# Kernel tuning notes

Hardware: AMD Instinct MI355X
Metric: run time of the kernel (lower is better)

The kernel has to match this reference:

```python
import jax, jax.numpy as jnp
import numpy as np

N_NODES = 50000
N_EDGES = 800000
D = 256          # in_features == out_features == num_classes
T = 4            # number of replicas / linear heads
NS = 64          # num_edges (hyperedges)


def setup_inputs() -> dict:
    key = jax.random.key(0)
    ks = jax.random.split(key, 10)
    s = D ** -0.5
    return {
        "edge_index": jax.random.randint(ks[0], (2, N_EDGES), 0, N_NODES, dtype=jnp.int64)
        if jax.config.jax_enable_x64 else jax.random.randint(ks[0], (2, N_EDGES), 0, N_NODES, dtype=jnp.int32),
        "features": jax.random.normal(ks[1], (N_NODES, D), jnp.float32),
        "lin_w": jax.random.normal(ks[2], (T, D, D), jnp.float32) * s,
        "lin_b": jax.random.normal(ks[3], (T, D), jnp.float32) * 0.01,
        "gcn0_w": jax.random.normal(ks[4], (D, D), jnp.float32) * s,
        "gcn0_b": jax.random.normal(ks[5], (D,), jnp.float32) * 0.01,
        "gcn1_w": jax.random.normal(ks[6], (D, D), jnp.float32) * s,
        "gcn1_b": jax.random.normal(ks[7], (D,), jnp.float32) * 0.01,
        "lin1_w": jax.random.normal(ks[8], (D, NS), jnp.float32) * s,
        "lin1_b": jax.random.normal(ks[9], (NS,), jnp.float32) * 0.01,
    }


def _l2_normalize(x, eps=1e-8):
    n = jnp.sqrt(jnp.sum(x * x, axis=-1, keepdims=True))
    return x / jnp.maximum(n, eps)


def reference(edge_index, features, lin_w, lin_b, gcn0_w, gcn0_b, gcn1_w, gcn1_b, lin1_w, lin1_b):
    num_nodes, d = features.shape
    t = lin_w.shape[0]
    ns = lin1_w.shape[1]
    scale = d ** -0.5  # out_features ** -0.5

    # t linear projections: (t, N, D)
    transformed = jnp.einsum('nd,tdk->tnk', features, lin_w) + lin_b[:, None, :]

    src, dst = edge_index[0], edge_index[1]
    # cosine similarity of features[src] vs each replica's transformed[dst]
    fs = _l2_normalize(features)[src]              # (E, D)
    tf_n = _l2_normalize(transformed)              # (t, N, D)
    sim = jnp.stack([jnp.sum(fs * tf_n[i][dst], axis=-1) for i in range(t)], axis=1)  # (E, t)
    best_idx = jnp.argmax(sim, axis=1)
    best_dst = dst + best_idx.astype(dst.dtype) * num_nodes

    # extra per-replica identity edges: node n -> node n + i*N, i in [0, t)
    ar = jnp.arange(num_nodes, dtype=src.dtype)
    extra_src = jnp.tile(ar, t)
    extra_dst = (ar[None, :] + (jnp.arange(t, dtype=src.dtype) * num_nodes)[:, None]).reshape(-1)

    src_all = jnp.concatenate([src, src, extra_src])
    dst_all = jnp.concatenate([dst, best_dst, extra_dst])
    n_total = (t + 1) * num_nodes

    # PyG gcn_norm: drop pre-existing self loops (weight 0), add one self loop per node,
    # symmetric normalization with degree from destination index.
    loops = jnp.arange(n_total, dtype=src.dtype)
    src2 = jnp.concatenate([src_all, loops])
    dst2 = jnp.concatenate([dst_all, loops])
    w2 = jnp.concatenate([jnp.where(src_all == dst_all, 0.0, 1.0).astype(features.dtype),
                          jnp.ones(n_total, features.dtype)])
    deg = jax.ops.segment_sum(w2, dst2, num_segments=n_total)
    dinv = jnp.where(deg > 0, jax.lax.rsqrt(deg), 0.0)
    norm = w2 * dinv[src2] * dinv[dst2]

    def gcn(x, W, b):
        xw = x @ W
        return jax.ops.segment_sum(norm[:, None] * xw[src2], dst2, num_segments=n_total) + b

    all_features = jnp.concatenate([features, transformed.reshape(t * num_nodes, d)], axis=0)
    # dropout is identity in eval mode
    h = jax.nn.relu(all_features)
    h = gcn(h, gcn0_w, gcn0_b)
    h = jax.nn.relu(h)
    all_features2 = gcn(h, gcn1_w, gcn1_b)          # ((t+1)N, D)
    logits = jax.nn.relu(all_features2) @ lin1_w + lin1_b  # ((t+1)N, NS)

    # H[n, c] counts how many of the (t+1) replicas assign node n to cluster c
    classes = jnp.argmax(logits.reshape(t + 1, num_nodes, ns), axis=-1)  # (t+1, N)
    H = jax.nn.one_hot(classes, ns, dtype=features.dtype).sum(axis=0)     # (N, NS)

    # hyperedge features: sum of all_features2 over base-replica nodes in each hyperedge
    mask = (H > 0).astype(features.dtype)                                  # (N, NS)
    hyperedge_features = mask.T @ all_features2[:num_nodes]                # (NS, D)

    dots = (all_features @ hyperedge_features.T) * scale                   # ((t+1)N, NS)
    return H, hyperedge_features, dots
```

## Files before the change

### kernel.cpp

```cpp
#include <hip/hip_runtime.h>

#define D 256
#define T 4
#define NS 64

typedef unsigned int uint32;
typedef short s16x8 __attribute__((ext_vector_type(8)));
typedef float f32x4 __attribute__((ext_vector_type(4)));

__device__ __forceinline__ float bflo(uint32 u) { return __uint_as_float(u << 16); }
__device__ __forceinline__ float bfhi(uint32 u) { return __uint_as_float(u & 0xffff0000u); }
__device__ __forceinline__ unsigned short f2bf(float x) {
    uint32 u = __float_as_uint(x);
    u = u + 0x7FFFu + ((u >> 16) & 1u);
    return (unsigned short)(u >> 16);
}
__device__ __forceinline__ uint32 pack2(float a, float b) {
    return (uint32)f2bf(a) | ((uint32)f2bf(b) << 16);
}
__device__ __forceinline__ uint32 relu2(uint32 u) {
    uint32 s = u & 0x80008000u;
    uint32 m = ((s >> 15) ^ 0x00010001u) * 0xFFFFu;
    return u & m;
}

__global__ void zero_kernel(uint32* __restrict__ p, long long n)
{
    long long i = (long long)blockIdx.x * blockDim.x + threadIdx.x;
    long long st = (long long)gridDim.x * blockDim.x;
    for (; i < n; i += st) p[i] = 0u;
}

__global__ void f2bf_kernel(const float* __restrict__ in, unsigned short* __restrict__ out,
                            long long n8)
{
    long long i = (long long)blockIdx.x * blockDim.x + threadIdx.x;
    long long st = (long long)gridDim.x * blockDim.x;
    for (; i < n8; i += st) {
        float4 a = *(const float4*)(in + i * 8);
        float4 b = *(const float4*)(in + i * 8 + 4);
        uint4 o;
        o.x = pack2(a.x, a.y); o.y = pack2(a.z, a.w);
        o.z = pack2(b.x, b.y); o.w = pack2(b.z, b.w);
        *(uint4*)(out + i * 8) = o;
    }
}

__global__ void wfrag_kernel(const float* __restrict__ g0, const float* __restrict__ g1,
                             const float* __restrict__ lw, unsigned short* __restrict__ out)
{
    int o = blockIdx.x * 256 + threadIdx.x;
    int mat = blockIdx.y;
    const float* W = (mat == 0) ? g0 : (mat == 1) ? g1 : (lw + (size_t)(mat - 2) * 65536);
    int j = o & 7, lane = (o >> 3) & 63, ks = (o >> 9) & 7, nt = o >> 12;
    int n15 = lane & 15, quad = lane >> 4;
    int k = ks * 32 + quad * 8 + j;
    int n = nt * 16 + n15;
    out[(size_t)mat * 65536 + o] = f2bf(W[(size_t)k * 256 + n]);
}

__global__ __launch_bounds__(256, 2)
void gemm_mfma(const unsigned short* __restrict__ A,
               const unsigned short* __restrict__ Wfrag,
               const float* __restrict__ bias,
               unsigned short* __restrict__ Cout,
               int M, int nStripes, int rowMul, int zRowAdd)
{
    __shared__ unsigned short Asm[64 * 264];
    int t = threadIdx.x, w = t >> 6, lane = t & 63;
    int n15 = lane & 15, quad = lane >> 4;
    int z = blockIdx.y;
    Wfrag += (size_t)z * 65536;
    bias  += (size_t)z * 256;

    s16x8 bfr[4][8];
#pragma unroll
    for (int nt = 0; nt < 4; nt++)
#pragma unroll
        for (int ks = 0; ks < 8; ks++)
            bfr[nt][ks] = *(const s16x8*)(Wfrag +
                (size_t)(((w * 4 + nt) * 8 + ks) * 64 + lane) * 8);

    float bcol[4];
#pragma unroll
    for (int nt = 0; nt < 4; nt++) bcol[nt] = bias[(w * 4 + nt) * 16 + n15];

    for (int s = blockIdx.x; s < nStripes; s += gridDim.x) {
        int m0 = s * 64;
        __syncthreads();
#pragma unroll
        for (int i = 0; i < 8; i++) {
            int idx = i * 256 + t;
            int m = idx >> 5, kc = (idx & 31) * 8;
            int gm = m0 + m;
            uint4 v = make_uint4(0u, 0u, 0u, 0u);
            if (gm < M) v = *(const uint4*)(A + (size_t)gm * 256 + kc);
            *(uint4*)(Asm + m * 264 + kc) = v;
        }
        __syncthreads();

        f32x4 acc[4][4];
#pragma unroll
        for (int rt = 0; rt < 4; rt++)
#pragma unroll
            for (int nt = 0; nt < 4; nt++)
#pragma unroll
                for (int e = 0; e < 4; e++) acc[rt][nt][e] = 0.f;

#pragma unroll
        for (int rt = 0; rt < 4; rt++) {
            int abase = (rt * 16 + n15) * 264 + quad * 8;
#pragma unroll
            for (int ks = 0; ks < 8; ks++) {
                s16x8 a = *(const s16x8*)(Asm + abase + ks * 32);
#pragma unroll
                for (int nt = 0; nt < 4; nt++)
                    acc[rt][nt] = __builtin_amdgcn_mfma_f32_16x16x32_bf16(
                        a, bfr[nt][ks], acc[rt][nt], 0, 0, 0);
            }
        }

#pragma unroll
        for (int rt = 0; rt < 4; rt++) {
            int row0 = m0 + rt * 16 + quad * 4;
#pragma unroll
            for (int nt = 0; nt < 4; nt++) {
                int colp = (w * 4 + nt) * 16 + n15;
#pragma unroll
                for (int r = 0; r < 4; r++) {
                    int gr = row0 + r;
                    if (gr < M) {
                        size_t ro = (size_t)gr * rowMul + (size_t)z * zRowAdd;
                        Cout[ro * 256 + colp] = f2bf(acc[rt][nt][r] + bcol[nt]);
                    }
                }
            }
        }
    }
}

__global__ __launch_bounds__(256)
void tinv_kernel(const unsigned short* __restrict__ tr, float* __restrict__ tinv, int rows)
{
    int wave = threadIdx.x >> 6, lane = threadIdx.x & 63;
    int r = blockIdx.x * 4 + wave;
    if (r >= rows) return;
    uint2 q = *(const uint2*)(tr + (size_t)r * D + lane * 4);
    float a = bflo(q.x), b = bfhi(q.x), c = bflo(q.y), d = bfhi(q.y);
    float s = a * a + b * b + c * c + d * d;
#pragma unroll
    for (int off = 32; off; off >>= 1) s += __shfl_xor(s, off);
    if (lane == 0) tinv[r] = 1.f / fmaxf(sqrtf(s), 1e-8f);
}

__global__ void ehist_kernel(const int* __restrict__ dst, int* __restrict__ ecnt, int E)
{
    for (int e = blockIdx.x * blockDim.x + threadIdx.x; e < E;
         e += gridDim.x * blockDim.x)
        atomicAdd(ecnt + dst[e], 1);
}

__global__ void escatter_kernel(const int* __restrict__ src, const int* __restrict__ dst,
                                const int* __restrict__ eptr, int* __restrict__ efill,
                                uint2* __restrict__ esorted, int E)
{
    for (int e = blockIdx.x * blockDim.x + threadIdx.x; e < E;
         e += gridDim.x * blockDim.x) {
        int d = dst[e];
        int pos = eptr[d] + atomicAdd(efill + d, 1);
        esorted[pos] = make_uint2((uint32)src[e], (uint32)d);
    }
}

__global__ __launch_bounds__(256)
void sim4_kernel(const uint2* __restrict__ esorted,
                 const unsigned short* __restrict__ featb,
                 const unsigned short* __restrict__ trI, const float* __restrict__ tinv,
                 int* __restrict__ bestS, int E, int Nn)
{
    int w = threadIdx.x >> 6, lane = threadIdx.x & 63;
    int n15 = lane & 15, quad = lane >> 4;
    int base = (blockIdx.x * 4 + w) * 16;
    if (base >= E) return;
    int ei = min(base + n15, E - 1);
    uint2 se = esorted[ei];
    const unsigned short* arow = featb + (size_t)se.x * D + quad * 8;
    const unsigned short* brow = trI + ((size_t)se.y * 4) * D + quad * 8;

    s16x8 a[8];
#pragma unroll
    for (int ks = 0; ks < 8; ks++) a[ks] = *(const s16x8*)(arow + ks * 32);

    f32x4 a0 = {0.f, 0.f, 0.f, 0.f}, a1 = a0, a2 = a0, a3 = a0;
#pragma unroll
    for (int ks = 0; ks < 8; ks++) {
        s16x8 b0 = *(const s16x8*)(brow + ks * 32);
        a0 = __builtin_amdgcn_mfma_f32_16x16x32_bf16(a[ks], b0, a0, 0, 0, 0);
    }
#pragma unroll
    for (int ks = 0; ks < 8; ks++) {
        s16x8 b1 = *(const s16x8*)(brow + D + ks * 32);
        a1 = __builtin_amdgcn_mfma_f32_16x16x32_bf16(a[ks], b1, a1, 0, 0, 0);
    }
#pragma unroll
    for (int ks = 0; ks < 8; ks++) {
        s16x8 b2 = *(const s16x8*)(brow + 2 * D + ks * 32);
        a2 = __builtin_amdgcn_mfma_f32_16x16x32_bf16(a[ks], b2, a2, 0, 0, 0);
    }
#pragma unroll
    for (int ks = 0; ks < 8; ks++) {
        s16x8 b3 = *(const s16x8*)(brow + 3 * D + ks * 32);
        a3 = __builtin_amdgcn_mfma_f32_16x16x32_bf16(a[ks], b3, a3, 0, 0, 0);
    }

    if (quad == (n15 >> 2) && base + n15 < E) {
        int r = n15 & 3;
        int d4 = (int)se.y * 4;
        float v0 = a0[r] * tinv[d4];
        float v1 = a1[r] * tinv[d4 + 1];
        float v2 = a2[r] * tinv[d4 + 2];
        float v3 = a3[r] * tinv[d4 + 3];
        float bv = v0; int bi = 0;
        if (v1 > bv) { bv = v1; bi = 1; }
        if (v2 > bv) { bv = v2; bi = 2; }
        if (v3 > bv) { bv = v3; bi = 3; }
        bestS[base + n15] = bi;
    }
}

__device__ __forceinline__ void decode_edge(int e, const uint2* __restrict__ esorted,
                                            const int* __restrict__ bestS,
                                            int E, int Nn, int& s, int& d, bool& keep)
{
    if (e < E) {
        uint2 se = esorted[e];
        s = (int)se.x; d = (int)se.y; keep = (s != d);
    } else if (e < 2 * E) {
        int k = e - E;
        uint2 se = esorted[k];
        s = (int)se.x; d = (int)se.y + bestS[k] * Nn; keep = (s != d);
    } else if (e < 2 * E + T * Nn) {
        int k = e - 2 * E; int i = k / Nn; int n = k - i * Nn;
        s = n; d = n + i * Nn; keep = (i != 0);
    } else {
        int v = e - (2 * E + T * Nn); s = v; d = v; keep = true;
    }
}

__global__ void hist_kernel(const uint2* __restrict__ esorted, const int* __restrict__ bestS,
                            int* __restrict__ cnt, int E, int Nn)
{
    int total = 2 * E + (2 * T + 1) * Nn;
    for (int e = blockIdx.x * blockDim.x + threadIdx.x; e < total;
         e += gridDim.x * blockDim.x) {
        int s, d; bool keep;
        decode_edge(e, esorted, bestS, E, Nn, s, d, keep);
        if (keep) atomicAdd(cnt + d, 1);
    }
}

__global__ void dinv_kernel(const int* __restrict__ cnt, float* __restrict__ dinv, int n)
{
    int v = blockIdx.x * blockDim.x + threadIdx.x;
    if (v < n) dinv[v] = (cnt[v] > 0) ? rsqrtf((float)cnt[v]) : 0.f;
}

__global__ void emeta_kernel(const uint2* __restrict__ esorted, const int* __restrict__ bestS,
                             const float* __restrict__ dinv, uint2* __restrict__ emeta, int E)
{
    for (int e = blockIdx.x * blockDim.x + threadIdx.x; e < E;
         e += gridDim.x * blockDim.x) {
        uint2 se = esorted[e];
        uint32 packed = se.x | ((uint32)bestS[e] << 27);
        emeta[e] = make_uint2(packed, __float_as_uint(dinv[se.x]));
    }
}

__global__ void scan_sums(const int* __restrict__ cnt, int* __restrict__ aux, int n)
{
    __shared__ int sd[256];
    int idx = blockIdx.x * 256 + threadIdx.x;
    sd[threadIdx.x] = (idx < n) ? cnt[idx] : 0;
    __syncthreads();
    for (int off = 128; off; off >>= 1) {
        if (threadIdx.x < off) sd[threadIdx.x] += sd[threadIdx.x + off];
        __syncthreads();
    }
    if (threadIdx.x == 0) aux[blockIdx.x] = sd[0];
}

__global__ void scan_aux(const int* __restrict__ aux, int* __restrict__ auxex, int nb)
{
    __shared__ int sd[1024];
    int t = threadIdx.x;
    int v = (t < nb) ? aux[t] : 0;
    sd[t] = v;
    __syncthreads();
    for (int off = 1; off < 1024; off <<= 1) {
        int x = (t >= off) ? sd[t - off] : 0;
        __syncthreads();
        sd[t] += x;
        __syncthreads();
    }
    if (t < nb) auxex[t] = sd[t] - v;
}

__global__ void scan_write(const int* __restrict__ cnt, const int* __restrict__ auxex,
                           int* __restrict__ rowptr, int n)
{
    __shared__ int sd[256];
    int t = threadIdx.x;
    int idx = blockIdx.x * 256 + t;
    int v = (idx < n) ? cnt[idx] : 0;
    sd[t] = v;
    __syncthreads();
    for (int off = 1; off < 256; off <<= 1) {
        int x = (t >= off) ? sd[t - off] : 0;
        __syncthreads();
        sd[t] += x;
        __syncthreads();
    }
    if (idx < n) {
        int rp = auxex[blockIdx.x] + sd[t] - v;
        rowptr[idx] = rp;
        if (idx == n - 1) rowptr[n] = rp + v;
    }
}

__global__ __launch_bounds__(256)
void agg5_kernel(const int* __restrict__ eptr, const uint2* __restrict__ emeta,
                 const unsigned short* __restrict__ xa,
                 const unsigned short* __restrict__ xb,
                 const float* __restrict__ dinv,
                 unsigned short* __restrict__ outb, int Nn, int xrm, int xra)
{
    int wave = threadIdx.x >> 6, lane = threadIdx.x & 63;
    int v = blockIdx.x * 4 + wave;
    if (v >= Nn) return;

    float dv  = dinv[v];
    float dr1 = dinv[v + Nn];
    float dr2 = dinv[v + 2 * Nn];
    float dr3 = dinv[v + 3 * Nn];
    float dr4 = dinv[v + 4 * Nn];

    uint2 qv = *(const uint2*)(xa + (size_t)v * D + lane * 4);
    qv.x = relu2(qv.x); qv.y = relu2(qv.y);
    float y0 = bflo(qv.x), y1 = bfhi(qv.x), y2 = bflo(qv.y), y3 = bfhi(qv.y);

    float wsb = dv * dv;
    float b0 = wsb * y0, b1 = wsb * y1, b2 = wsb * y2, b3 = wsb * y3;

    float wi1 = dv * dr1, wi2 = dv * dr2, wi3 = dv * dr3;
    float r10 = wi1 * y0, r11 = wi1 * y1, r12 = wi1 * y2, r13 = wi1 * y3;
    float r20 = wi2 * y0, r21 = wi2 * y1, r22 = wi2 * y2, r23 = wi2 * y3;
    float r30 = wi3 * y0, r31 = wi3 * y1, r32 = wi3 * y2, r33 = wi3 * y3;
    float r40 = 0.f, r41 = 0.f, r42 = 0.f, r43 = 0.f;

    {
        uint2 q = *(const uint2*)(xb + ((size_t)v * xrm + 0 * (size_t)xra) * D + lane * 4);
        q.x = relu2(q.x); q.y = relu2(q.y);
        float ws = dr1 * dr1;
        r10 = fmaf(ws, bflo(q.x), r10); r11 = fmaf(ws, bfhi(q.x), r11);
        r12 = fmaf(ws, bflo(q.y), r12); r13 = fmaf(ws, bfhi(q.y), r13);
    }
    {
        uint2 q = *(const uint2*)(xb + ((size_t)v * xrm + 1 * (size_t)xra) * D + lane * 4);
        q.x = relu2(q.x); q.y = relu2(q.y);
        float ws = dr2 * dr2;
        r20 = fmaf(ws, bflo(q.x), r20); r21 = fmaf(ws, bfhi(q.x), r21);
        r22 = fmaf(ws, bflo(q.y), r22); r23 = fmaf(ws, bfhi(q.y), r23);
    }
    {
        uint2 q = *(const uint2*)(xb + ((size_t)v * xrm + 2 * (size_t)xra) * D + lane * 4);
        q.x = relu2(q.x); q.y = relu2(q.y);
        float ws = dr3 * dr3;
        r30 = fmaf(ws, bflo(q.x), r30); r31 = fmaf(ws, bfhi(q.x), r31);
        r32 = fmaf(ws, bflo(q.y), r32); r33 = fmaf(ws, bfhi(q.y), r33);
    }
    {
        uint2 q = *(const uint2*)(xb + ((size_t)v * xrm + 3 * (size_t)xra) * D + lane * 4);
        q.x = relu2(q.x); q.y = relu2(q.y);
        float ws = dr4 * dr4;
        r40 = fmaf(ws, bflo(q.x), r40); r41 = fmaf(ws, bfhi(q.x), r41);
        r42 = fmaf(ws, bflo(q.y), r42); r43 = fmaf(ws, bfhi(q.y), r43);
    }

    int j = eptr[v], jend = eptr[v + 1];

#define EDGE_BODY(qq, ss, bb, ww)                                                  \
    {                                                                              \
        float x0 = bflo(qq.x), x1 = bfhi(qq.x), x2 = bflo(qq.y), x3 = bfhi(qq.y);  \
        float wb = (ss != v) ? (ww) * dv : 0.f;                                    \
        if (bb == 0) wb += wb;                                                     \
        b0 = fmaf(wb, x0, b0); b1 = fmaf(wb, x1, b1);                              \
        b2 = fmaf(wb, x2, b2); b3 = fmaf(wb, x3, b3);                              \
        if (bb == 1) {                                                             \
            float wr = (ww) * dr1;                                                 \
            r10 = fmaf(wr, x0, r10); r11 = fmaf(wr, x1, r11);                      \
            r12 = fmaf(wr, x2, r12); r13 = fmaf(wr, x3, r13);                      \
        } else if (bb == 2) {                                                      \
            float wr = (ww) * dr2;                                                 \
            r20 = fmaf(wr, x0, r20); r21 = fmaf(wr, x1, r21);                      \
            r22 = fmaf(wr, x2, r22); r23 = fmaf(wr, x3, r23);                      \
        } else if (bb == 3) {                                                      \
            float wr = (ww) * dr3;                                                 \
            r30 = fmaf(wr, x0, r30); r31 = fmaf(wr, x1, r31);                      \
            r32 = fmaf(wr, x2, r32); r33 = fmaf(wr, x3, r33);                      \
        }                                                                          \
    }

    for (; j + 2 <= jend; j += 2) {
        uint2 m0 = emeta[j];
        uint2 m1 = emeta[j + 1];
        uint32 su0 = (uint32)__builtin_amdgcn_readfirstlane((int)m0.x);
        uint32 su1 = (uint32)__builtin_amdgcn_readfirstlane((int)m1.x);
        float ws0 = __uint_as_float((uint32)__builtin_amdgcn_readfirstlane((int)m0.y));
        float ws1 = __uint_as_float((uint32)__builtin_amdgcn_readfirstlane((int)m1.y));
        int s0 = (int)(su0 & 0x07FFFFFFu), bx0 = (int)(su0 >> 27);
        int s1 = (int)(su1 & 0x07FFFFFFu), bx1 = (int)(su1 >> 27);
        uint2 q0 = *(const uint2*)(xa + (size_t)s0 * D + lane * 4);
        uint2 q1 = *(const uint2*)(xa + (size_t)s1 * D + lane * 4);
        q0.x = relu2(q0.x); q0.y = relu2(q0.y);
        q1.x = relu2(q1.x); q1.y = relu2(q1.y);
        EDGE_BODY(q0, s0, bx0, ws0);
        EDGE_BODY(q1, s1, bx1, ws1);
    }
    if (j < jend) {
        uint2 m0 = emeta[j];
        uint32 su0 = (uint32)__builtin_amdgcn_readfirstlane((int)m0.x);
        float ws0 = __uint_as_float((uint32)__builtin_amdgcn_readfirstlane((int)m0.y));
        int s0 = (int)(su0 & 0x07FFFFFFu), bx0 = (int)(su0 >> 27);
        uint2 q0 = *(const uint2*)(xa + (size_t)s0 * D + lane * 4);
        q0.x = relu2(q0.x); q0.y = relu2(q0.y);
        EDGE_BODY(q0, s0, bx0, ws0);
    }
#undef EDGE_BODY

    uint2 o;
    o.x = pack2(b0, b1); o.y = pack2(b2, b3);
    *(uint2*)(outb + (size_t)v * D + lane * 4) = o;
    o.x = pack2(r10, r11); o.y = pack2(r12, r13);
    *(uint2*)(outb + ((size_t)v + Nn) * D + lane * 4) = o;
    o.x = pack2(r20, r21); o.y = pack2(r22, r23);
    *(uint2*)(outb + ((size_t)v + 2 * (size_t)Nn) * D + lane * 4) = o;
    o.x = pack2(r30, r31); o.y = pack2(r32, r33);
    *(uint2*)(outb + ((size_t)v + 3 * (size_t)Nn) * D + lane * 4) = o;
    o.x = pack2(r40, r41); o.y = pack2(r42, r43);
    *(uint2*)(outb + ((size_t)v + 4 * (size_t)Nn) * D + lane * 4) = o;
}

__global__ __launch_bounds__(256, 2)
void logits_mfma(const unsigned short* __restrict__ af2, const float* __restrict__ Wl,
                 const float* __restrict__ bl, float* __restrict__ H,
                 int M, int Nn, int nStripes)
{
    __shared__ unsigned short Asm[64 * 264];
    int t = threadIdx.x, w = t >> 6, lane = t & 63;
    int n15 = lane & 15, quad = lane >> 4;

    s16x8 bfr[4][8];
#pragma unroll
    for (int nt = 0; nt < 4; nt++)
#pragma unroll
        for (int ks = 0; ks < 8; ks++) {
            s16x8 f;
#pragma unroll
            for (int j = 0; j < 8; j++) {
                int k = ks * 32 + quad * 8 + j;
                f[j] = (short)f2bf(Wl[(size_t)k * NS + nt * 16 + n15]);
            }
            bfr[nt][ks] = f;
        }
    float bcol[4];
#pragma unroll
    for (int nt = 0; nt < 4; nt++) bcol[nt] = bl[nt * 16 + n15];

    for (int s = blockIdx.x; s < nStripes; s += gridDim.x) {
        int m0 = s * 64;
        __syncthreads();
#pragma unroll
        for (int i = 0; i < 8; i++) {
            int idx = i * 256 + t;
            int m = idx >> 5, kc = (idx & 31) * 8;
            int gm = m0 + m;
            uint4 v = make_uint4(0u, 0u, 0u, 0u);
            if (gm < M) {
                v = *(const uint4*)(af2 + (size_t)gm * 256 + kc);
                v.x = relu2(v.x); v.y = relu2(v.y);
                v.z = relu2(v.z); v.w = relu2(v.w);
            }
            *(uint4*)(Asm + m * 264 + kc) = v;
        }
        __syncthreads();

        f32x4 acc[4];
#pragma unroll
        for (int nt = 0; nt < 4; nt++)
#pragma unroll
            for (int e = 0; e < 4; e++) acc[nt][e] = 0.f;

        int abase = (w * 16 + n15) * 264 + quad * 8;
#pragma unroll
        for (int ks = 0; ks < 8; ks++) {
            s16x8 a = *(const s16x8*)(Asm + abase + ks * 32);
#pragma unroll
            for (int nt = 0; nt < 4; nt++)
                acc[nt] = __builtin_amdgcn_mfma_f32_16x16x32_bf16(
                    a, bfr[nt][ks], acc[nt], 0, 0, 0);
        }

#pragma unroll
        for (int e = 0; e < 4; e++) {
            float bv = acc[0][e] + bcol[0]; int bi = n15;
#pragma unroll
            for (int nt = 1; nt < 4; nt++) {
                float v = acc[nt][e] + bcol[nt];
                int c = nt * 16 + n15;
                if (v > bv) { bv = v; bi = c; }
            }
#pragma unroll
            for (int off = 1; off < 16; off <<= 1) {
                float ov = __shfl_xor(bv, off);
                int   oi = __shfl_xor(bi, off);
                if (ov > bv || (ov == bv && oi < bi)) { bv = ov; bi = oi; }
            }
            if (n15 == 0) {
                int gr = m0 + w * 16 + quad * 4 + e;
                if (gr < M) atomicAdd(H + (size_t)(gr % Nn) * NS + bi, 1.0f);
            }
        }
    }
}

__global__ __launch_bounds__(256)
void maskTb_kernel(const float* __restrict__ H, unsigned short* __restrict__ maskTb,
                   int Nn, int Kpad)
{
    __shared__ unsigned short tile[64 * 72];
    int t = threadIdx.x;
    int n0 = blockIdx.x * 64;
    int c = t & 63, rr = t >> 6;
#pragma unroll
    for (int i = 0; i < 16; i++) {
        int n = rr + i * 4;
        float hv = (n0 + n < Nn) ? H[(size_t)(n0 + n) * NS + c] : 0.f;
        tile[c * 72 + n] = (hv > 0.f) ? (unsigned short)0x3F80 : (unsigned short)0;
    }
    __syncthreads();
#pragma unroll
    for (int i = 0; i < 2; i++) {
        int idx = i * 256 + t;
        int cc = idx >> 3, ch = idx & 7;
        uint4 v = *(const uint4*)(tile + cc * 72 + ch * 8);
        *(uint4*)(maskTb + (size_t)cc * Kpad + n0 + ch * 8) = v;
    }
}

__global__ __launch_bounds__(256, 2)
void he_gemm(const unsigned short* __restrict__ maskTb,
             const unsigned short* __restrict__ af2,
             float* __restrict__ partials, int Kpad)
{
    __shared__ unsigned short Bsm[32 * 264];
    int t = threadIdx.x, w = t >> 6, lane = t & 63;
    int n15 = lane & 15, quad = lane >> 4;
    int k0 = blockIdx.x * 256;

    f32x4 acc[4][4];
#pragma unroll
    for (int mt = 0; mt < 4; mt++)
#pragma unroll
        for (int nt = 0; nt < 4; nt++)
#pragma unroll
            for (int e = 0; e < 4; e++) acc[mt][nt][e] = 0.f;

    for (int s = 0; s < 8; s++) {
        int k = k0 + s * 32;
        __syncthreads();
#pragma unroll
        for (int i = 0; i < 4; i++) {
            int idx = i * 256 + t;
            int row = idx >> 5, col8 = (idx & 31) * 8;
            uint4 v = *(const uint4*)(af2 + (size_t)(k + row) * 256 + col8);
            *(uint4*)(Bsm + row * 264 + col8) = v;
        }
        __syncthreads();

        s16x8 a[4];
#pragma unroll
        for (int mt = 0; mt < 4; mt++)
            a[mt] = *(const s16x8*)(maskTb + (size_t)(mt * 16 + n15) * Kpad
                                    + k + quad * 8);
#pragma unroll
        for (int nt = 0; nt < 4; nt++) {
            int ncol = w * 64 + nt * 16 + n15;
            s16x8 b;
#pragma unroll
            for (int j = 0; j < 8; j++)
                b[j] = (short)Bsm[(quad * 8 + j) * 264 + ncol];
#pragma unroll
            for (int mt = 0; mt < 4; mt++)
                acc[mt][nt] = __builtin_amdgcn_mfma_f32_16x16x32_bf16(
                    a[mt], b, acc[mt][nt], 0, 0, 0);
        }
    }

    float* pdst = partials + (size_t)blockIdx.x * (64 * 256);
#pragma unroll
    for (int mt = 0; mt < 4; mt++)
#pragma unroll
        for (int nt = 0; nt < 4; nt++)
#pragma unroll
            for (int r = 0; r < 4; r++) {
                int m = mt * 16 + quad * 4 + r;
                int n = w * 64 + nt * 16 + n15;
                pdst[(size_t)m * 256 + n] = acc[mt][nt][r];
            }
}

__global__ __launch_bounds__(256)
void he_reduce2(const float* __restrict__ partials, float* __restrict__ he, int KB)
{
    int idx = blockIdx.x * 256 + threadIdx.x;
    float s = 0.f;
    for (int b = 0; b < KB; b++)
        s += partials[(size_t)b * 16384 + idx];
    he[idx] = s;
}

__global__ void bigb_copy(const float* __restrict__ he, float* __restrict__ BigB)
{
    int idx = blockIdx.x * 256 + threadIdx.x;
    if (idx < D * NS) {
        int d = idx >> 6, c = idx & 63;
        BigB[idx] = he[(size_t)c * D + d];
    }
}

__global__ __launch_bounds__(256)
void bigb_mm(const float* __restrict__ lin_w, const float* __restrict__ lin_b,
             const float* __restrict__ he, float* __restrict__ BigB,
             float* __restrict__ beta)
{
    int gw = (int)((blockIdx.x * 256 + threadIdx.x) >> 6);
    int lane = threadIdx.x & 63;
    const int totalA = T * D * NS;
    if (gw >= totalA + T * NS) return;
    const float* xrow; const float* hrow; float* outp;
    if (gw < totalA) {
        int t = gw / (D * NS); int rem = gw - t * D * NS;
        int d = rem / NS; int c = rem - d * NS;
        xrow = lin_w + ((size_t)t * D + d) * D;
        hrow = he + (size_t)c * D;
        outp = BigB + ((size_t)(t + 1) * D + d) * NS + c;
    } else {
        int i = gw - totalA; int t = i / NS; int c = i - t * NS;
        xrow = lin_b + (size_t)t * D;
        hrow = he + (size_t)c * D;
        outp = beta + (size_t)(t + 1) * NS + c;
    }
    float4 x = *(const float4*)(xrow + lane * 4);
    float4 h = *(const float4*)(hrow + lane * 4);
    float s = x.x * h.x + x.y * h.y + x.z * h.z + x.w * h.w;
#pragma unroll
    for (int off = 32; off; off >>= 1) s += __shfl_xor(s, off);
    if (lane == 0) *outp = s;
}

__global__ __launch_bounds__(256, 2)
void dots_mfma(const unsigned short* __restrict__ featb,
               const float* __restrict__ feat32, int useBf,
               const float* __restrict__ BigB,
               const float* __restrict__ beta, float* __restrict__ dots,
               int Nn, int nStripes)
{
    __shared__ unsigned short Asm[64 * 264];
    int t = threadIdx.x, w = t >> 6, lane = t & 63;
    int n15 = lane & 15, quad = lane >> 4;
    int rho = blockIdx.y;
    const float* Bp = BigB + (size_t)rho * D * NS;

    s16x8 bfr[4][8];
#pragma unroll
    for (int nt = 0; nt < 4; nt++)
#pragma unroll
        for (int ks = 0; ks < 8; ks++) {
            s16x8 f;
#pragma unroll
            for (int j = 0; j < 8; j++) {
                int k = ks * 32 + quad * 8 + j;
                f[j] = (short)f2bf(Bp[(size_t)k * NS + nt * 16 + n15]);
            }
            bfr[nt][ks] = f;
        }
    float bcol[4];
#pragma unroll
    for (int nt = 0; nt < 4; nt++) bcol[nt] = beta[rho * NS + nt * 16 + n15];

    for (int s = blockIdx.x; s < nStripes; s += gridDim.x) {
        int m0 = s * 64;
        __syncthreads();
#pragma unroll
        for (int i = 0; i < 8; i++) {
            int idx = i * 256 + t;
            int m = idx >> 5, kc = (idx & 31) * 8;
            int gm = m0 + m;
            uint4 o = make_uint4(0u, 0u, 0u, 0u);
            if (gm < Nn) {
                if (useBf) {
                    o = *(const uint4*)(featb + (size_t)gm * 256 + kc);
                } else {
                    float4 a = *(const float4*)(feat32 + (size_t)gm * 256 + kc);
                    float4 b = *(const float4*)(feat32 + (size_t)gm * 256 + kc + 4);
                    o.x = pack2(a.x, a.y); o.y = pack2(a.z, a.w);
                    o.z = pack2(b.x, b.y); o.w = pack2(b.z, b.w);
                }
            }
            *(uint4*)(Asm + m * 264 + kc) = o;
        }
        __syncthreads();

        f32x4 acc[4];
#pragma unroll
        for (int nt = 0; nt < 4; nt++)
#pragma unroll
            for (int e = 0; e < 4; e++) acc[nt][e] = 0.f;

        int abase = (w * 16 + n15) * 264 + quad * 8;
#pragma unroll
        for (int ks = 0; ks < 8; ks++) {
            s16x8 a = *(const s16x8*)(Asm + abase + ks * 32);
#pragma unroll
            for (int nt = 0; nt < 4; nt++)
                acc[nt] = __builtin_amdgcn_mfma_f32_16x16x32_bf16(
                    a, bfr[nt][ks], acc[nt], 0, 0, 0);
        }

#pragma unroll
        for (int e = 0; e < 4; e++) {
            int gr = m0 + w * 16 + quad * 4 + e;
            if (gr >= Nn) continue;
#pragma unroll
            for (int nt = 0; nt < 4; nt++) {
                int c = nt * 16 + n15;
                dots[((size_t)rho * Nn + gr) * NS + c] = (acc[nt][e] + bcol[nt]) * 0.0625f;
            }
        }
    }
}

extern "C" void kernel_launch(void* const* d_in, const int* in_sizes, int n_in,
                              void* d_out, int out_size, void* d_ws, size_t ws_size,
                              hipStream_t stream)
{
    const int*   edge_index = (const int*)d_in[0];
    const float* features   = (const float*)d_in[1];
    const float* lin_w      = (const float*)d_in[2];
    const float* lin_b      = (const float*)d_in[3];
    const float* gcn0_w     = (const float*)d_in[4];
    const float* gcn0_b     = (const float*)d_in[5];
    const float* gcn1_w     = (const float*)d_in[6];
    const float* gcn1_b     = (const float*)d_in[7];
    const float* lin1_w     = (const float*)d_in[8];
    const float* lin1_b     = (const float*)d_in[9];

    int E  = in_sizes[0] / 2;
    int Nn = in_sizes[1] / D;
    int n_total = (T + 1) * Nn;
    int Mrep = T * Nn;

    const int* src = edge_index;
    const int* dst = edge_index + E;

    float* out_H    = (float*)d_out;
    float* out_he   = out_H + (size_t)Nn * NS;
    float* out_dots = out_he + (size_t)NS * D;

    int KB   = (Nn + 255) / 256;
    int Kpad = KB * 256;

    char* ws0 = (char*)d_ws;
    char* wsp = ws0;
    auto carve = [&](size_t bytes) {
        char* p = wsp; wsp += (bytes + 255) & ~(size_t)255; return p;
    };
    unsigned short* R1   = (unsigned short*)carve((size_t)n_total * D * 2);
    unsigned short* R2   = (unsigned short*)carve((size_t)n_total * D * 2);
    float*          BigB = (float*)carve((size_t)(T + 1) * D * NS * 4);
    float*          beta = (float*)carve((size_t)(T + 1) * NS * 4);
    unsigned short* trI  = R2;

    size_t featb_bytes = (size_t)Nn * D * 2;
    unsigned short* featb = nullptr;
    int useBfDots = 0;
    if ((size_t)(wsp - ws0) + featb_bytes + 256 <= ws_size) {
        featb = (unsigned short*)carve(featb_bytes);
        useBfDots = 1;
    }

    char* sc = (char*)out_dots;
    auto carve2 = [&](size_t bytes) {
        char* p = sc; sc += (bytes + 255) & ~(size_t)255; return p;
    };
    float* tinv    = (float*)carve2((size_t)Mrep * 4);
    int*   best    = (int*)carve2((size_t)E * 4);
    int*   cnt     = (int*)carve2((size_t)n_total * 4);
    float* dinv    = (float*)carve2((size_t)n_total * 4);
    int*   aux     = (int*)carve2(1024 * 4);
    int*   auxex   = (int*)carve2(1024 * 4);
    if (!featb) featb = (unsigned short*)carve2(featb_bytes);
    unsigned short* Wfrags = (unsigned short*)carve2((size_t)6 * 65536 * 2);
    int*   ecnt    = (int*)carve2((size_t)Nn * 4);
    int*   eptr    = (int*)carve2((size_t)(Nn + 1) * 4);
    int*   efill   = (int*)carve2((size_t)Nn * 4);
    uint2* esorted = (uint2*)carve2((size_t)E * 8);
    uint2* emeta   = (uint2*)carve2((size_t)E * 8);
    unsigned short* maskTb = (unsigned short*)carve2((size_t)NS * Kpad * 2);

    float* partials = (float*)R1;

    zero_kernel<<<512, 256, 0, stream>>>((uint32*)cnt, n_total);
    zero_kernel<<<512, 256, 0, stream>>>((uint32*)ecnt, Nn);
    zero_kernel<<<512, 256, 0, stream>>>((uint32*)efill, Nn);
    zero_kernel<<<512, 256, 0, stream>>>((uint32*)out_H, (long long)Nn * NS + NS * D);
    zero_kernel<<<1, 256, 0, stream>>>((uint32*)beta, (T + 1) * NS);

    wfrag_kernel<<<dim3(256, 6), 256, 0, stream>>>(gcn0_w, gcn1_w, lin_w, Wfrags);
    f2bf_kernel<<<2048, 256, 0, stream>>>(features, featb, (long long)Nn * D / 8);

    int strN = (Nn + 63) / 64;
    gemm_mfma<<<dim3(512, T), 256, 0, stream>>>(featb, Wfrags + 2 * 65536, lin_b,
                                                trI, Nn, strN, T, 1);
    tinv_kernel<<<(Mrep + 3) / 4, 256, 0, stream>>>(trI, tinv, Mrep);

    ehist_kernel<<<2048, 256, 0, stream>>>(dst, ecnt, E);
    int enb = (Nn + 255) / 256;
    scan_sums<<<enb, 256, 0, stream>>>(ecnt, aux, Nn);
    scan_aux<<<1, 1024, 0, stream>>>(aux, auxex, enb);
    scan_write<<<enb, 256, 0, stream>>>(ecnt, auxex, eptr, Nn);
    escatter_kernel<<<2048, 256, 0, stream>>>(src, dst, eptr, efill, esorted, E);
    int nGroups = (E + 15) / 16;
    sim4_kernel<<<(nGroups + 3) / 4, 256, 0, stream>>>(esorted, featb, trI,
                                                       tinv, best, E, Nn);

    hist_kernel<<<2048, 256, 0, stream>>>(esorted, best, cnt, E, Nn);
    dinv_kernel<<<(n_total + 255) / 256, 256, 0, stream>>>(cnt, dinv, n_total);
    emeta_kernel<<<2048, 256, 0, stream>>>(esorted, best, dinv, emeta, E);

    int strT = (n_total + 63) / 64;
    agg5_kernel<<<(Nn + 3) / 4, 256, 0, stream>>>(eptr, emeta, featb, trI,
                                                  dinv, R1, Nn, 4, 1);
    gemm_mfma<<<dim3(512, 1), 256, 0, stream>>>(R1, Wfrags, gcn0_b, R1, n_total,
                                                strT, 1, 0);

    agg5_kernel<<<(Nn + 3) / 4, 256, 0, stream>>>(eptr, emeta, R1, R1 + (size_t)Nn * D,
                                                  dinv, R2, Nn, 1, Nn);
    gemm_mfma<<<dim3(512, 1), 256, 0, stream>>>(R2, Wfrags + 65536, gcn1_b, R2,
                                                n_total, strT, 1, 0);

    logits_mfma<<<512, 256, 0, stream>>>(R2, lin1_w, lin1_b, out_H, n_total, Nn, strT);

    maskTb_kernel<<<Kpad / 64, 256, 0, stream>>>(out_H, maskTb, Nn, Kpad);
    he_gemm<<<KB, 256, 0, stream>>>(maskTb, R2, partials, Kpad);
    he_reduce2<<<64, 256, 0, stream>>>(partials, out_he, KB);

    bigb_copy<<<(D * NS + 255) / 256, 256, 0, stream>>>(out_he, BigB);
    bigb_mm<<<(T * D * NS + T * NS + 3) / 4, 256, 0, stream>>>(lin_w, lin_b, out_he,
                                                               BigB, beta);
    dots_mfma<<<dim3(160, 5), 256, 0, stream>>>(featb, features, useBfDots,
                                                BigB, beta, out_dots, Nn, strN);
}
```

Measured before the change: 1.016 ms.

## Fuse norm and dinv kernels, switch transformed layout, unroll aggregation by four

Computes the inverse L2 norms of the transformed rows inside the projection GEMM epilogue and drops the separate tinv kernel. Changes the transformed tensor from node-interleaved to replica-major layout, fuses the dinv computation into the emeta kernel, and merges three zero launches into one contiguous buffer. Adds a 4-edge unrolled path in the aggregation loop to keep more gathers in flight. The new layout spreads each node's four replica rows far apart for the similarity gathers, and the epilogue adds LDS atomics and extra syncs.

```diff
diff --git a/kernel.cpp b/kernel.cpp
--- a/kernel.cpp
+++ b/kernel.cpp
@@ -64,9 +64,11 @@
                const unsigned short* __restrict__ Wfrag,
                const float* __restrict__ bias,
                unsigned short* __restrict__ Cout,
-               int M, int nStripes, int rowMul, int zRowAdd)
+               int M, int nStripes, int rowMul, int zRowAdd,
+               float* __restrict__ tinvOut)
 {
     __shared__ unsigned short Asm[64 * 264];
+    __shared__ float rn[64];
     int t = threadIdx.x, w = t >> 6, lane = t & 63;
     int n15 = lane & 15, quad = lane >> 4;
     int z = blockIdx.y;
@@ -136,21 +138,36 @@
                 }
             }
         }
-    }
-}
-
-__global__ __launch_bounds__(256)
-void tinv_kernel(const unsigned short* __restrict__ tr, float* __restrict__ tinv, int rows)
-{
-    int wave = threadIdx.x >> 6, lane = threadIdx.x & 63;
-    int r = blockIdx.x * 4 + wave;
-    if (r >= rows) return;
-    uint2 q = *(const uint2*)(tr + (size_t)r * D + lane * 4);
-    float a = bflo(q.x), b = bfhi(q.x), c = bflo(q.y), d = bfhi(q.y);
-    float s = a * a + b * b + c * c + d * d;
-#pragma unroll
-    for (int off = 32; off; off >>= 1) s += __shfl_xor(s, off);
-    if (lane == 0) tinv[r] = 1.f / fmaxf(sqrtf(s), 1e-8f);
+
+        if (tinvOut) {
+            if (t < 64) rn[t] = 0.f;
+            __syncthreads();
+#pragma unroll
+            for (int rt = 0; rt < 4; rt++)
+#pragma unroll
+                for (int r = 0; r < 4; r++) {
+                    float p = 0.f;
+#pragma unroll
+                    for (int nt = 0; nt < 4; nt++) {
+                        uint32 ub = ((uint32)f2bf(acc[rt][nt][r] + bcol[nt])) << 16;
+                        float vv = __uint_as_float(ub);
+                        p += vv * vv;
+                    }
+#pragma unroll
+                    for (int off = 1; off < 16; off <<= 1) p += __shfl_xor(p, off);
+                    if (n15 == 0)
+                        atomicAdd(&rn[rt * 16 + quad * 4 + r], p);
+                }
+            __syncthreads();
+            if (t < 64) {
+                int gr2 = m0 + t;
+                if (gr2 < M) {
+                    size_t ro2 = (size_t)gr2 * rowMul + (size_t)z * zRowAdd;
+                    tinvOut[ro2] = 1.f / fmaxf(sqrtf(rn[t]), 1e-8f);
+                }
+            }
+        }
+    }
 }
 
 __global__ void ehist_kernel(const int* __restrict__ dst, int* __restrict__ ecnt, int E)
@@ -175,7 +192,7 @@
 __global__ __launch_bounds__(256)
 void sim4_kernel(const uint2* __restrict__ esorted,
                  const unsigned short* __restrict__ featb,
-                 const unsigned short* __restrict__ trI, const float* __restrict__ tinv,
+                 const unsigned short* __restrict__ tr, const float* __restrict__ tinv,
                  int* __restrict__ bestS, int E, int Nn)
 {
     int w = threadIdx.x >> 6, lane = threadIdx.x & 63;
@@ -185,7 +202,8 @@
     int ei = min(base + n15, E - 1);
     uint2 se = esorted[ei];
     const unsigned short* arow = featb + (size_t)se.x * D + quad * 8;
-    const unsigned short* brow = trI + ((size_t)se.y * 4) * D + quad * 8;
+    const unsigned short* brow = tr + (size_t)se.y * D + quad * 8;
+    size_t rstride = (size_t)Nn * D;
 
     s16x8 a[8];
 #pragma unroll
@@ -199,27 +217,27 @@
     }
 #pragma unroll
     for (int ks = 0; ks < 8; ks++) {
-        s16x8 b1 = *(const s16x8*)(brow + D + ks * 32);
+        s16x8 b1 = *(const s16x8*)(brow + rstride + ks * 32);
         a1 = __builtin_amdgcn_mfma_f32_16x16x32_bf16(a[ks], b1, a1, 0, 0, 0);
     }
 #pragma unroll
     for (int ks = 0; ks < 8; ks++) {
-        s16x8 b2 = *(const s16x8*)(brow + 2 * D + ks * 32);
+        s16x8 b2 = *(const s16x8*)(brow + 2 * rstride + ks * 32);
         a2 = __builtin_amdgcn_mfma_f32_16x16x32_bf16(a[ks], b2, a2, 0, 0, 0);
     }
 #pragma unroll
     for (int ks = 0; ks < 8; ks++) {
-        s16x8 b3 = *(const s16x8*)(brow + 3 * D + ks * 32);
+        s16x8 b3 = *(const s16x8*)(brow + 3 * rstride + ks * 32);
         a3 = __builtin_amdgcn_mfma_f32_16x16x32_bf16(a[ks], b3, a3, 0, 0, 0);
     }
 
     if (quad == (n15 >> 2) && base + n15 < E) {
         int r = n15 & 3;
-        int d4 = (int)se.y * 4;
-        float v0 = a0[r] * tinv[d4];
-        float v1 = a1[r] * tinv[d4 + 1];
-        float v2 = a2[r] * tinv[d4 + 2];
-        float v3 = a3[r] * tinv[d4 + 3];
+        int d = (int)se.y;
+        float v0 = a0[r] * tinv[d];
+        float v1 = a1[r] * tinv[Nn + d];
+        float v2 = a2[r] * tinv[2 * Nn + d];
+        float v3 = a3[r] * tinv[3 * Nn + d];
         float bv = v0; int bi = 0;
         if (v1 > bv) { bv = v1; bi = 1; }
         if (v2 > bv) { bv = v2; bi = 2; }
@@ -259,20 +277,24 @@
     }
 }
 
-__global__ void dinv_kernel(const int* __restrict__ cnt, float* __restrict__ dinv, int n)
-{
-    int v = blockIdx.x * blockDim.x + threadIdx.x;
-    if (v < n) dinv[v] = (cnt[v] > 0) ? rsqrtf((float)cnt[v]) : 0.f;
-}
-
-__global__ void emeta_kernel(const uint2* __restrict__ esorted, const int* __restrict__ bestS,
-                             const float* __restrict__ dinv, uint2* __restrict__ emeta, int E)
-{
-    for (int e = blockIdx.x * blockDim.x + threadIdx.x; e < E;
-         e += gridDim.x * blockDim.x) {
-        uint2 se = esorted[e];
-        uint32 packed = se.x | ((uint32)bestS[e] << 27);
-        emeta[e] = make_uint2(packed, __float_as_uint(dinv[se.x]));
+__global__ void emeta_dinv_kernel(const uint2* __restrict__ esorted,
+                                  const int* __restrict__ bestS,
+                                  const int* __restrict__ cnt,
+                                  float* __restrict__ dinv, uint2* __restrict__ emeta,
+                                  int E, int n_total, int work)
+{
+    for (int i = blockIdx.x * blockDim.x + threadIdx.x; i < work;
+         i += gridDim.x * blockDim.x) {
+        if (i < n_total) {
+            int c = cnt[i];
+            dinv[i] = (c > 0) ? rsqrtf((float)c) : 0.f;
+        }
+        if (i < E) {
+            uint2 se = esorted[i];
+            uint32 packed = se.x | ((uint32)bestS[i] << 27);
+            float dv = rsqrtf((float)cnt[se.x]);
+            emeta[i] = make_uint2(packed, __float_as_uint(dv));
+        }
     }
 }
 
@@ -387,6 +409,10 @@
     }
 
     int j = eptr[v], jend = eptr[v + 1];
+
+#define EDGE_META(mm, ssu, wws)                                                    \
+    uint32 ssu = (uint32)__builtin_amdgcn_readfirstlane((int)mm.x);                \
+    float wws = __uint_as_float((uint32)__builtin_amdgcn_readfirstlane((int)mm.y));
 
 #define EDGE_BODY(qq, ss, bb, ww)                                                  \
     {                                                                              \
@@ -410,13 +436,34 @@
         }                                                                          \
     }
 
+    for (; j + 4 <= jend; j += 4) {
+        uint2 m0 = emeta[j];
+        uint2 m1 = emeta[j + 1];
+        uint2 m2 = emeta[j + 2];
+        uint2 m3 = emeta[j + 3];
+        EDGE_META(m0, su0, ws0); EDGE_META(m1, su1, ws1);
+        EDGE_META(m2, su2, ws2); EDGE_META(m3, su3, ws3);
+        int s0 = (int)(su0 & 0x07FFFFFFu), bx0 = (int)(su0 >> 27);
+        int s1 = (int)(su1 & 0x07FFFFFFu), bx1 = (int)(su1 >> 27);
+        int s2 = (int)(su2 & 0x07FFFFFFu), bx2 = (int)(su2 >> 27);
+        int s3 = (int)(su3 & 0x07FFFFFFu), bx3 = (int)(su3 >> 27);
+        uint2 q0 = *(const uint2*)(xa + (size_t)s0 * D + lane * 4);
+        uint2 q1 = *(const uint2*)(xa + (size_t)s1 * D + lane * 4);
+        uint2 q2 = *(const uint2*)(xa + (size_t)s2 * D + lane * 4);
+        uint2 q3 = *(const uint2*)(xa + (size_t)s3 * D + lane * 4);
+        q0.x = relu2(q0.x); q0.y = relu2(q0.y);
+        q1.x = relu2(q1.x); q1.y = relu2(q1.y);
+        q2.x = relu2(q2.x); q2.y = relu2(q2.y);
+        q3.x = relu2(q3.x); q3.y = relu2(q3.y);
+        EDGE_BODY(q0, s0, bx0, ws0);
+        EDGE_BODY(q1, s1, bx1, ws1);
+        EDGE_BODY(q2, s2, bx2, ws2);
+        EDGE_BODY(q3, s3, bx3, ws3);
+    }
     for (; j + 2 <= jend; j += 2) {
         uint2 m0 = emeta[j];
         uint2 m1 = emeta[j + 1];
-        uint32 su0 = (uint32)__builtin_amdgcn_readfirstlane((int)m0.x);
-        uint32 su1 = (uint32)__builtin_amdgcn_readfirstlane((int)m1.x);
-        float ws0 = __uint_as_float((uint32)__builtin_amdgcn_readfirstlane((int)m0.y));
-        float ws1 = __uint_as_float((uint32)__builtin_amdgcn_readfirstlane((int)m1.y));
+        EDGE_META(m0, su0, ws0); EDGE_META(m1, su1, ws1);
         int s0 = (int)(su0 & 0x07FFFFFFu), bx0 = (int)(su0 >> 27);
         int s1 = (int)(su1 & 0x07FFFFFFu), bx1 = (int)(su1 >> 27);
         uint2 q0 = *(const uint2*)(xa + (size_t)s0 * D + lane * 4);
@@ -428,14 +475,14 @@
     }
     if (j < jend) {
         uint2 m0 = emeta[j];
-        uint32 su0 = (uint32)__builtin_amdgcn_readfirstlane((int)m0.x);
-        float ws0 = __uint_as_float((uint32)__builtin_amdgcn_readfirstlane((int)m0.y));
+        EDGE_META(m0, su0, ws0);
         int s0 = (int)(su0 & 0x07FFFFFFu), bx0 = (int)(su0 >> 27);
         uint2 q0 = *(const uint2*)(xa + (size_t)s0 * D + lane * 4);
         q0.x = relu2(q0.x); q0.y = relu2(q0.y);
         EDGE_BODY(q0, s0, bx0, ws0);
     }
 #undef EDGE_BODY
+#undef EDGE_META
 
     uint2 o;
     o.x = pack2(b0, b1); o.y = pack2(b2, b3);
@@ -789,7 +836,7 @@
     unsigned short* R2   = (unsigned short*)carve((size_t)n_total * D * 2);
     float*          BigB = (float*)carve((size_t)(T + 1) * D * NS * 4);
     float*          beta = (float*)carve((size_t)(T + 1) * NS * 4);
-    unsigned short* trI  = R2;
+    unsigned short* transformed = R2;
 
     size_t featb_bytes = (size_t)Nn * D * 2;
     unsigned short* featb = nullptr;
@@ -805,24 +852,22 @@
     };
     float* tinv    = (float*)carve2((size_t)Mrep * 4);
     int*   best    = (int*)carve2((size_t)E * 4);
-    int*   cnt     = (int*)carve2((size_t)n_total * 4);
+    int*   cnt     = (int*)carve2((size_t)(n_total + 2 * Nn) * 4);
+    int*   ecnt    = cnt + n_total;
+    int*   efill   = ecnt + Nn;
     float* dinv    = (float*)carve2((size_t)n_total * 4);
     int*   aux     = (int*)carve2(1024 * 4);
     int*   auxex   = (int*)carve2(1024 * 4);
     if (!featb) featb = (unsigned short*)carve2(featb_bytes);
     unsigned short* Wfrags = (unsigned short*)carve2((size_t)6 * 65536 * 2);
-    int*   ecnt    = (int*)carve2((size_t)Nn * 4);
     int*   eptr    = (int*)carve2((size_t)(Nn + 1) * 4);
-    int*   efill   = (int*)carve2((size_t)Nn * 4);
     uint2* esorted = (uint2*)carve2((size_t)E * 8);
     uint2* emeta   = (uint2*)carve2((size_t)E * 8);
     unsigned short* maskTb = (unsigned short*)carve2((size_t)NS * Kpad * 2);
 
     float* partials = (float*)R1;
 
-    zero_kernel<<<512, 256, 0, stream>>>((uint32*)cnt, n_total);
-    zero_kernel<<<512, 256, 0, stream>>>((uint32*)ecnt, Nn);
-    zero_kernel<<<512, 256, 0, stream>>>((uint32*)efill, Nn);
+    zero_kernel<<<512, 256, 0, stream>>>((uint32*)cnt, (long long)(n_total + 2 * Nn));
     zero_kernel<<<512, 256, 0, stream>>>((uint32*)out_H, (long long)Nn * NS + NS * D);
     zero_kernel<<<1, 256, 0, stream>>>((uint32*)beta, (T + 1) * NS);
 
@@ -831,8 +876,7 @@
 
     int strN = (Nn + 63) / 64;
     gemm_mfma<<<dim3(512, T), 256, 0, stream>>>(featb, Wfrags + 2 * 65536, lin_b,
-                                                trI, Nn, strN, T, 1);
-    tinv_kernel<<<(Mrep + 3) / 4, 256, 0, stream>>>(trI, tinv, Mrep);
+                                                transformed, Nn, strN, 1, Nn, tinv);
 
     ehist_kernel<<<2048, 256, 0, stream>>>(dst, ecnt, E);
     int enb = (Nn + 255) / 256;
@@ -841,23 +885,24 @@
     scan_write<<<enb, 256, 0, stream>>>(ecnt, auxex, eptr, Nn);
     escatter_kernel<<<2048, 256, 0, stream>>>(src, dst, eptr, efill, esorted, E);
     int nGroups = (E + 15) / 16;
-    sim4_kernel<<<(nGroups + 3) / 4, 256, 0, stream>>>(esorted, featb, trI,
+    sim4_kernel<<<(nGroups + 3) / 4, 256, 0, stream>>>(esorted, featb, transformed,
                                                        tinv, best, E, Nn);
 
     hist_kernel<<<2048, 256, 0, stream>>>(esorted, best, cnt, E, Nn);
-    dinv_kernel<<<(n_total + 255) / 256, 256, 0, stream>>>(cnt, dinv, n_total);
-    emeta_kernel<<<2048, 256, 0, stream>>>(esorted, best, dinv, emeta, E);
+    int work = (E > n_total) ? E : n_total;
+    emeta_dinv_kernel<<<2048, 256, 0, stream>>>(esorted, best, cnt, dinv, emeta,
+                                                E, n_total, work);
 
     int strT = (n_total + 63) / 64;
-    agg5_kernel<<<(Nn + 3) / 4, 256, 0, stream>>>(eptr, emeta, featb, trI,
-                                                  dinv, R1, Nn, 4, 1);
+    agg5_kernel<<<(Nn + 3) / 4, 256, 0, stream>>>(eptr, emeta, featb, transformed,
+                                                  dinv, R1, Nn, 1, Nn);
     gemm_mfma<<<dim3(512, 1), 256, 0, stream>>>(R1, Wfrags, gcn0_b, R1, n_total,
-                                                strT, 1, 0);
+                                                strT, 1, 0, nullptr);
 
     agg5_kernel<<<(Nn + 3) / 4, 256, 0, stream>>>(eptr, emeta, R1, R1 + (size_t)Nn * D,
                                                   dinv, R2, Nn, 1, Nn);
     gemm_mfma<<<dim3(512, 1), 256, 0, stream>>>(R2, Wfrags + 65536, gcn1_b, R2,
-                                                n_total, strT, 1, 0);
+                                                n_total, strT, 1, 0, nullptr);
 
     logits_mfma<<<512, 256, 0, stream>>>(R2, lin1_w, lin1_b, out_H, n_total, Nn, strT);
 
```

Result: faster. 987.8 us (-2.7%).
